# Performance work log

Measured on AMD Instinct MI355X. Metric: run time of the kernel, lower is better.

The kernel has to match this reference:

```python
import jax, jax.numpy as jnp
import numpy as np

HIDDEN = 1024
ATT_FEAT = 2048
EMBED = 512


def setup_inputs() -> dict:
    key = jax.random.key(0)
    k1, k2, k3, k4, k5, k6 = jax.random.split(key, 6)
    B, S, N = 16, 64, 196
    hidden = jax.random.normal(k1, (B, S, HIDDEN), dtype=jnp.float32)
    feats = jax.random.normal(k2, (B, N, ATT_FEAT), dtype=jnp.float32)
    att_mask = jax.random.randint(k3, (B, N), 0, 2, dtype=jnp.int32)
    # parameters (scaled like default torch Linear init)
    w_h = jax.random.normal(k4, (HIDDEN, EMBED), dtype=jnp.float32) / np.sqrt(HIDDEN)
    w_u = jax.random.normal(k5, (ATT_FEAT, EMBED), dtype=jnp.float32) / np.sqrt(ATT_FEAT)
    b = jnp.ones((EMBED,), dtype=jnp.float32)
    w = jax.random.normal(k6, (EMBED,), dtype=jnp.float32) / np.sqrt(EMBED)
    return {"hidden": hidden, "feats": feats, "att_mask": att_mask,
            "w_h": w_h, "w_u": w_u, "b": b, "w": w}


def reference(hidden, feats, att_mask, w_h, w_u, b, w):
    # hidden: [B,S,H], feats: [B,N,F], att_mask: [B,N]
    Wh = jnp.einsum('bsh,he->bse', hidden, w_h)          # [B,S,E]
    Uv = jnp.einsum('bnf,fe->bne', feats, w_u)           # [B,N,E] (feats repeat is redundant; same math)
    # additive attention energies: tanh(Wh + Uv + b) . w  -> [B,S,N]
    e = jnp.tanh(Wh[:, :, None, :] + Uv[:, None, :, :] + b)
    scores = jnp.einsum('bsne,e->bsn', e, w)             # [B,S,N]
    scores = jnp.where(att_mask[:, None, :] == 0, jnp.float32(-1e9), scores)
    weights = jax.nn.softmax(scores, axis=-1)            # [B,S,N]
    attn_feats = jnp.einsum('bsn,bnf->bsf', weights, feats)  # [B,S,F]
    return attn_feats, weights
```

## Files before the change

kernel.cpp:

```cpp
#include <hip/hip_runtime.h>
#include <math.h>

#define BATCH 16
#define SEQ 64
#define NKEY 196
#define NPAD 224
#define HIDDEN 1024
#define ATT_FEAT 2048
#define EMBED 512
#define MPAD 3200

using half8    = __attribute__((ext_vector_type(8))) _Float16;
using half4    = __attribute__((ext_vector_type(4))) _Float16;
using f32x4    = __attribute__((ext_vector_type(4))) float;
using f32x16   = __attribute__((ext_vector_type(16))) float;
using float4v  = __attribute__((ext_vector_type(4))) float;

#define KCONST (-2.8853900817779268f)
#define LOG2E  (1.4426950408889634f)

__device__ __forceinline__ void gl_lds16(const _Float16* g, _Float16* l) {
    __builtin_amdgcn_global_load_lds(
        (const __attribute__((address_space(1))) unsigned int*)g,
        (__attribute__((address_space(3))) unsigned int*)l, 16, 0, 0);
}

__device__ inline void prep_a128(
    const float* __restrict__ A, _Float16* __restrict__ T,
    int K, int Mreal, int tm, int tk, int t)
{
    const int r  = t >> 1;
    const int hf = t & 1;
    const int grow = tm * 128 + r;
    float f[32];
    if (grow < Mreal) {
        const float* src = A + (size_t)grow * K + tk * 64 + hf * 32;
        #pragma unroll
        for (int q = 0; q < 8; ++q) {
            float4v v = *(const float4v*)(src + q * 4);
            f[q*4+0] = v.x; f[q*4+1] = v.y; f[q*4+2] = v.z; f[q*4+3] = v.w;
        }
    } else {
        #pragma unroll
        for (int j = 0; j < 32; ++j) f[j] = 0.f;
    }
    const int tkk = tk * 2 + hf;
    const size_t base = ((size_t)tm * (K >> 5) + tkk) * 4096;
    #pragma unroll
    for (int s = 0; s < 2; ++s)
        #pragma unroll
        for (int kh = 0; kh < 2; ++kh) {
            half8 h;
            #pragma unroll
            for (int j = 0; j < 8; ++j)
                h[j] = (_Float16)f[s * 16 + kh * 8 + j];
            *(half8*)(T + base + (size_t)((s * 2 + kh) * 128 + r) * 8) = h;
        }
}

__device__ inline void prep_b128(
    const float* __restrict__ W, _Float16* __restrict__ T,
    int K, int N, int tn, int tk, int t, float (*tile)[129])
{
    {
        const int kr = t >> 2;
        const int nc = (t & 3) * 32;
        const float* src = W + (size_t)(tk * 64 + kr) * N + tn * 128 + nc;
        #pragma unroll
        for (int q = 0; q < 8; ++q) {
            float4v v = *(const float4v*)(src + q * 4);
            tile[kr][nc + q*4 + 0] = v.x; tile[kr][nc + q*4 + 1] = v.y;
            tile[kr][nc + q*4 + 2] = v.z; tile[kr][nc + q*4 + 3] = v.w;
        }
    }
    __syncthreads();
    {
        const int c  = t >> 1;
        const int hf = t & 1;
        const int tkk = tk * 2 + hf;
        const size_t base = ((size_t)tn * (K >> 5) + tkk) * 4096;
        #pragma unroll
        for (int s = 0; s < 2; ++s)
            #pragma unroll
            for (int kh = 0; kh < 2; ++kh) {
                half8 h;
                #pragma unroll
                for (int j = 0; j < 8; ++j)
                    h[j] = (_Float16)tile[hf * 32 + s * 16 + kh * 8 + j][c];
                *(half8*)(T + base + (size_t)((s * 2 + kh) * 128 + c) * 8) = h;
            }
    }
}

__device__ inline void prep_bT(
    const float* __restrict__ Wb, _Float16* __restrict__ T,
    int tn, int tk, int t, float (*tile)[129])
{
    {
        const int kr = t >> 2;
        const int nc = (t & 3) * 32;
        const int gn = tk * 64 + kr;
        #pragma unroll
        for (int q = 0; q < 8; ++q) {
            float4v v = {0.f, 0.f, 0.f, 0.f};
            if (gn < NKEY)
                v = *(const float4v*)(Wb + (size_t)gn * ATT_FEAT + tn * 128 + nc + q * 4);
            tile[kr][nc + q*4 + 0] = v.x; tile[kr][nc + q*4 + 1] = v.y;
            tile[kr][nc + q*4 + 2] = v.z; tile[kr][nc + q*4 + 3] = v.w;
        }
    }
    __syncthreads();
    {
        const int c  = t >> 1;
        const int hf = t & 1;
        const int tkk = tk * 2 + hf;
        if (tkk < 7) {
            const size_t base = ((size_t)tn * 7 + tkk) * 4096;
            #pragma unroll
            for (int s = 0; s < 2; ++s)
                #pragma unroll
                for (int kh = 0; kh < 2; ++kh) {
                    half8 h;
                    #pragma unroll
                    for (int j = 0; j < 8; ++j)
                        h[j] = (_Float16)tile[hf * 32 + s * 16 + kh * 8 + j][c];
                    *(half8*)(T + base + (size_t)((s * 2 + kh) * 128 + c) * 8) = h;
                }
        }
    }
}

__global__ __launch_bounds__(256) void uber_prep(
    const float* __restrict__ hidden, const float* __restrict__ feats,
    const float* __restrict__ w_h, const float* __restrict__ w_u,
    _Float16* HA, _Float16* FA, _Float16* HB, _Float16* UB)
{
    __shared__ float tile[64][129];
    const int id = blockIdx.x;
    const int t  = threadIdx.x;
    if (id < 128) {
        prep_a128(hidden, HA, HIDDEN, BATCH * SEQ, id >> 4, id & 15, t);
    } else if (id < 928) {
        const int j = id - 128;
        prep_a128(feats, FA, ATT_FEAT, BATCH * NKEY, j >> 5, j & 31, t);
    } else if (id < 992) {
        const int j = id - 928;
        prep_b128(w_h, HB, HIDDEN, EMBED, j >> 4, j & 15, t, tile);
    } else {
        const int j = id - 992;
        prep_b128(w_u, UB, ATT_FEAT, EMBED, j >> 5, j & 31, t, tile);
    }
}

__global__ __launch_bounds__(256) void uber_gemm(
    const _Float16* __restrict__ HA, const _Float16* __restrict__ HB,
    const _Float16* __restrict__ FA, const _Float16* __restrict__ UB,
    const float* __restrict__ bvec, _Float16* __restrict__ WhP,
    _Float16* __restrict__ UvP)
{
    __shared__ __align__(16) _Float16 L[2][3][4096];

    const int hh = blockIdx.x;
    const int t0 = (hh & 7) * 58 + (hh >> 3);

    const _Float16 *Aimg, *Bimg;
    const float* bias = nullptr;
    _Float16* C;
    int rt, ct, tk0, aK;
    if (t0 < 400) {
        const int ks = t0 / 100, rem = t0 % 100;
        rt = rem >> 2; ct = rem & 3;
        Aimg = FA; Bimg = UB;
        aK = ATT_FEAT >> 5; tk0 = ks * 16;
        C = UvP + (size_t)ks * MPAD * EMBED;
        if (ks == 0) bias = bvec;
    } else {
        const int v = t0 - 400;
        const int ks = v >> 5, rem = v & 31;
        rt = rem >> 2; ct = rem & 3;
        Aimg = HA; Bimg = HB;
        aK = HIDDEN >> 5; tk0 = ks * 16;
        C = WhP + (size_t)ks * (BATCH * SEQ) * EMBED;
    }

    const int tid = threadIdx.x, lane = tid & 63, w = tid >> 6;
    const int wr = w >> 1, wc = w & 1;
    const int l31 = lane & 31, kh = lane >> 5;

    const int isB = w >> 1;
    const int whf = w & 1;
    const _Float16* srcMat = isB ? Bimg : Aimg;
    const int majorTile = isB ? ct : rt;
    const _Float16* src0 =
        srcMat + ((size_t)majorTile * aK + tk0) * 4096 + whf * 2048 + lane * 8;

    f32x16 acc[2][2] = {};

    auto stage = [&](int buf, int t) {
        const _Float16* s = src0 + (size_t)t * 4096;
        _Float16* d = &L[isB][buf][0] + whf * 2048 + lane * 8;
        #pragma unroll
        for (int c = 0; c < 4; ++c)
            gl_lds16(s + c * 512, d + c * 512);
    };

    auto compute = [&](int buf) {
        #pragma unroll
        for (int s = 0; s < 2; ++s) {
            const int rb = (s * 2 + kh) * 128;
            half8 a[2], b[2];
            #pragma unroll
            for (int m = 0; m < 2; ++m)
                a[m] = *(const half8*)&L[0][buf][(rb + wr * 64 + m * 32 + l31) * 8];
            #pragma unroll
            for (int n = 0; n < 2; ++n)
                b[n] = *(const half8*)&L[1][buf][(rb + wc * 64 + n * 32 + l31) * 8];
            __builtin_amdgcn_s_setprio(1);
            #pragma unroll
            for (int m = 0; m < 2; ++m)
                #pragma unroll
                for (int n = 0; n < 2; ++n)
                    acc[m][n] = __builtin_amdgcn_mfma_f32_32x32x16_f16(a[m], b[n], acc[m][n], 0, 0, 0);
            __builtin_amdgcn_s_setprio(0);
        }
    };

    stage(0, 0); stage(1, 1);
    int cur = 0, nxt = 2;
    #pragma unroll 1
    for (int t = 0; t < 16; ++t) {
        if (t + 1 < 16) asm volatile("s_waitcnt vmcnt(4)" ::: "memory");
        else            asm volatile("s_waitcnt vmcnt(0)" ::: "memory");
        __builtin_amdgcn_s_barrier();
        if (t + 2 < 16) stage(nxt, t + 2);
        __builtin_amdgcn_sched_barrier(0);
        compute(cur);
        __builtin_amdgcn_sched_barrier(0);
        cur = (cur == 2) ? 0 : cur + 1;
        nxt = (nxt == 2) ? 0 : nxt + 1;
    }

    #pragma unroll
    for (int m = 0; m < 2; ++m) {
        const int row0 = rt * 128 + wr * 64 + m * 32;
        #pragma unroll
        for (int n = 0; n < 2; ++n) {
            const int colg = ct * 128 + wc * 64 + n * 32 + l31;
            const float bv = bias ? bias[colg] : 0.f;
            #pragma unroll
            for (int r = 0; r < 16; ++r) {
                const int row = (r & 3) + 8 * (r >> 2) + 4 * kh;
                C[(size_t)(row0 + row) * EMBED + colg] =
                    (_Float16)((acc[m][n][r] + bv) * KCONST);
            }
        }
    }
}

__global__ __launch_bounds__(256) void scores_ft(
    const _Float16* __restrict__ WhP, const _Float16* __restrict__ UvP,
    const float* __restrict__ wvec, const float* __restrict__ feats,
    float* __restrict__ scr4, _Float16* __restrict__ FT)
{
    __shared__ __align__(16) char smem[64 * 129 * 4];
    const int id = blockIdx.x;
    const int tid = threadIdx.x;

    if (id >= 832) {
        const int j = id - 832;
        const int b = j >> 6, rem = j & 63;
        prep_bT(feats + (size_t)b * NKEY * ATT_FEAT,
                FT + (size_t)b * 16 * 7 * 4096, rem >> 2, rem & 3, tid,
                (float(*)[129])smem);
        return;
    }

    const int n0 = (id % 13) * 16;
    const int eq = (id / 13) & 3;
    const int b  = id / 52;
    const int w    = tid >> 6;
    const int lane = tid & 63;

    float* whs = (float*)smem;
    float (*uvs)[64] = (float(*)[64])(smem + 16384);

    const size_t WHS = (size_t)(BATCH * SEQ) * EMBED;
    const size_t UVS = (size_t)MPAD * EMBED;

    float acc[4] = {};
    char* whsB = (char*)whs;

    for (int ch = 0; ch < 2; ++ch) {
        const int e0 = eq * 128 + ch * 64;
        {
            const int r = tid >> 2;
            const _Float16* Wr = WhP + (size_t)(b * SEQ + r) * EMBED + e0 + (tid & 3) * 16;
            half8 h0 = *(const half8*)(Wr);
            half8 h1 = *(const half8*)(Wr + 8);
            half8 g0 = *(const half8*)(Wr + WHS);
            half8 g1 = *(const half8*)(Wr + WHS + 8);
            float f[16];
            #pragma unroll
            for (int j = 0; j < 8; ++j) {
                f[j]     = (float)h0[j] + (float)g0[j];
                f[8 + j] = (float)h1[j] + (float)g1[j];
            }
            #pragma unroll
            for (int q = 0; q < 4; ++q) {
                const int cc = (tid & 3) * 16 + q * 4;
                float4v v = { f[q*4+0], f[q*4+1], f[q*4+2], f[q*4+3] };
                *(float4v*)(whsB + r * 256 + ((cc * 4) ^ ((r & 15) << 4))) = v;
            }
        }
        {
            const int nl = tid >> 4;
            const int c4 = tid & 15;
            const int nr = (n0 + nl < NKEY) ? (n0 + nl) : (NKEY - 1);
            const _Float16* Ur = UvP + (size_t)(b * NKEY + nr) * EMBED + e0 + c4 * 4;
            half4 u0 = *(const half4*)(Ur);
            half4 u1 = *(const half4*)(Ur + UVS);
            half4 u2 = *(const half4*)(Ur + 2 * UVS);
            half4 u3 = *(const half4*)(Ur + 3 * UVS);
            float4v u;
            u.x = ((float)u0[0] + (float)u1[0]) + ((float)u2[0] + (float)u3[0]);
            u.y = ((float)u0[1] + (float)u1[1]) + ((float)u2[1] + (float)u3[1]);
            u.z = ((float)u0[2] + (float)u1[2]) + ((float)u2[2] + (float)u3[2]);
            u.w = ((float)u0[3] + (float)u1[3]) + ((float)u2[3] + (float)u3[3]);
            *(float4v*)&uvs[nl][c4 * 4] = u;
        }
        __syncthreads();

        #pragma unroll
        for (int ec = 0; ec < 8; ++ec) {
            const int sb = lane * 256;
            float4v wh0 = *(const float4v*)(whsB + sb + ((ec * 32 +  0) ^ ((lane & 15) << 4)));
            float4v wh1 = *(const float4v*)(whsB + sb + ((ec * 32 + 16) ^ ((lane & 15) << 4)));
            float wf[8];
            #pragma unroll
            for (int i = 0; i < 8; ++i) wf[i] = wvec[e0 + ec * 8 + i];
            #pragma unroll
            for (int j = 0; j < 4; ++j) {
                const int nl = w * 4 + j;
                float4v u0 = *(const float4v*)&uvs[nl][ec * 8];
                float4v u1 = *(const float4v*)&uvs[nl][ec * 8 + 4];
                float t0 = __builtin_amdgcn_exp2f(wh0.x + u0.x);
                float t1 = __builtin_amdgcn_exp2f(wh0.y + u0.y);
                float t2 = __builtin_amdgcn_exp2f(wh0.z + u0.z);
                float t3 = __builtin_amdgcn_exp2f(wh0.w + u0.w);
                float t4 = __builtin_amdgcn_exp2f(wh1.x + u1.x);
                float t5 = __builtin_amdgcn_exp2f(wh1.y + u1.y);
                float t6 = __builtin_amdgcn_exp2f(wh1.z + u1.z);
                float t7 = __builtin_amdgcn_exp2f(wh1.w + u1.w);
                float a = acc[j];
                a = fmaf(wf[0], __builtin_amdgcn_rcpf(1.f + t0), a);
                a = fmaf(wf[1], __builtin_amdgcn_rcpf(1.f + t1), a);
                a = fmaf(wf[2], __builtin_amdgcn_rcpf(1.f + t2), a);
                a = fmaf(wf[3], __builtin_amdgcn_rcpf(1.f + t3), a);
                a = fmaf(wf[4], __builtin_amdgcn_rcpf(1.f + t4), a);
                a = fmaf(wf[5], __builtin_amdgcn_rcpf(1.f + t5), a);
                a = fmaf(wf[6], __builtin_amdgcn_rcpf(1.f + t6), a);
                a = fmaf(wf[7], __builtin_amdgcn_rcpf(1.f + t7), a);
                acc[j] = a;
            }
        }
        __syncthreads();
    }

    float* dst = scr4 + ((size_t)eq * (BATCH * SEQ) + b * SEQ + lane) * NKEY;
    #pragma unroll
    for (int j = 0; j < 4; ++j) {
        const int n = n0 + w * 4 + j;
        if (n < NKEY) dst[n] = 2.f * acc[j];
    }
}

__global__ __launch_bounds__(256) void attn_mfma(
    const float* __restrict__ scr4, const int* __restrict__ mask,
    const _Float16* __restrict__ FT,
    float* __restrict__ weights_out, float* __restrict__ out)
{
    const int fb = blockIdx.x;
    const int b  = blockIdx.y;
    const int t  = threadIdx.x;
    const int lane = t & 63, w = t >> 6;
    const int wr = w >> 1, wc = w & 1;
    const int l31 = lane & 31, khl = lane >> 5;

    __shared__ __align__(16) _Float16 wtL[7 * 4 * 64 * 8];
    __shared__ __align__(16) _Float16 Lb[3][4096];

    const _Float16* FTb = FT + (size_t)b * 16 * 7 * 4096 + (size_t)fb * 7 * 4096;

    auto stage = [&](int buf, int kt) {
        const _Float16* s = FTb + (size_t)kt * 4096 + w * 1024 + lane * 8;
        _Float16* d = &Lb[buf][0] + w * 1024 + lane * 8;
        gl_lds16(s, d);
        gl_lds16(s + 512, d + 512);
    };

    stage(0, 0); stage(1, 1);

    #pragma unroll
    for (int i = 0; i < 7; ++i)
        *(half8*)&wtL[(i * 256 + t) * 8] = (half8)(_Float16)0.f;

    asm volatile("s_waitcnt lgkmcnt(0)" ::: "memory");
    __builtin_amdgcn_s_barrier();

    {
        const int r  = t >> 2;
        const int ln = t & 3;
        const size_t SCRS = (size_t)(BATCH * SEQ) * NKEY;
        const float* p = scr4 + (size_t)(b * SEQ + r) * NKEY;
        const int* mrow = mask + b * NKEY;
        float v[49];
        float mx = -INFINITY;
        #pragma unroll
        for (int j = 0; j < 49; ++j) {
            const int n = ln + 4 * j;
            float s = (p[n] + p[SCRS + n]) + (p[2 * SCRS + n] + p[3 * SCRS + n]);
            if (mrow[n] == 0) s = -1e9f;
            v[j] = s;
            mx = fmaxf(mx, s);
        }
        mx = fmaxf(mx, __shfl_xor(mx, 1));
        mx = fmaxf(mx, __shfl_xor(mx, 2));
        float sum = 0.f;
        #pragma unroll
        for (int j = 0; j < 49; ++j) {
            v[j] = __builtin_amdgcn_exp2f((v[j] - mx) * LOG2E);
            sum += v[j];
        }
        sum += __shfl_xor(sum, 1);
        sum += __shfl_xor(sum, 2);
        const float inv = __builtin_amdgcn_rcpf(sum);
        float* wrow = weights_out + (size_t)(b * SEQ + r) * NKEY;
        #pragma unroll
        for (int j = 0; j < 49; ++j) {
            const int n = ln + 4 * j;
            const float wv = v[j] * inv;
            if (fb == 0) wrow[n] = wv;
            const int grp = ((n >> 4) & 1) * 2 + ((n >> 3) & 1);
            wtL[(((n >> 5) * 4 + grp) * 64 + r) * 8 + (n & 7)] = (_Float16)wv;
        }
    }
    asm volatile("s_waitcnt lgkmcnt(0)" ::: "memory");

    f32x16 acc[2] = {};
    #pragma unroll 1
    for (int kt = 0; kt < 7; ++kt) {
        if (kt < 6) asm volatile("s_waitcnt vmcnt(2)" ::: "memory");
        else        asm volatile("s_waitcnt vmcnt(0)" ::: "memory");
        __builtin_amdgcn_s_barrier();
        if (kt + 2 < 7) stage((kt + 2) % 3, kt + 2);
        __builtin_amdgcn_sched_barrier(0);
        const int buf = kt % 3;
        #pragma unroll
        for (int ks = 0; ks < 2; ++ks) {
            half8 a = *(const half8*)&wtL[(((kt * 4) + ks * 2 + khl) * 64 + wr * 32 + l31) * 8];
            half8 b0 = *(const half8*)&Lb[buf][((ks * 2 + khl) * 128 + wc * 64 + l31) * 8];
            half8 b1 = *(const half8*)&Lb[buf][((ks * 2 + khl) * 128 + wc * 64 + 32 + l31) * 8];
            acc[0] = __builtin_amdgcn_mfma_f32_32x32x16_f16(a, b0, acc[0], 0, 0, 0);
            acc[1] = __builtin_amdgcn_mfma_f32_32x32x16_f16(a, b1, acc[1], 0, 0, 0);
        }
        __builtin_amdgcn_sched_barrier(0);
    }

    #pragma unroll
    for (int nf = 0; nf < 2; ++nf) {
        const int f = fb * 128 + wc * 64 + nf * 32 + l31;
        #pragma unroll
        for (int r = 0; r < 16; ++r) {
            const int srow = wr * 32 + (r & 3) + 8 * (r >> 2) + 4 * khl;
            out[(size_t)(b * SEQ + srow) * ATT_FEAT + f] = acc[nf][r];
        }
    }
}

extern "C" void kernel_launch(void* const* d_in, const int* in_sizes, int n_in,
                              void* d_out, int out_size, void* d_ws, size_t ws_size,
                              hipStream_t stream)
{
    const float* hidden = (const float*)d_in[0];
    const float* feats  = (const float*)d_in[1];
    const int*   mask   = (const int*)  d_in[2];
    const float* w_h    = (const float*)d_in[3];
    const float* w_u    = (const float*)d_in[4];
    const float* bvec   = (const float*)d_in[5];
    const float* wvec   = (const float*)d_in[6];

    float* out         = (float*)d_out;
    float* attn_out    = out;
    float* weights_out = out + (size_t)BATCH * SEQ * ATT_FEAT;

    _Float16* WhP = (_Float16*)d_ws;
    _Float16* UvP = WhP + (size_t)2 * BATCH * SEQ * EMBED;
    float*    scr4 = (float*)(UvP + (size_t)4 * MPAD * EMBED);
    _Float16* FA = (_Float16*)(scr4 + (size_t)4 * BATCH * SEQ * NKEY);
    _Float16* HA = FA + (size_t)MPAD * ATT_FEAT;
    _Float16* UB = HA + (size_t)BATCH * SEQ * HIDDEN;
    _Float16* HB = UB + (size_t)EMBED * ATT_FEAT;
    _Float16* FT = HB + (size_t)EMBED * HIDDEN;

    uber_prep<<<dim3(1120), 256, 0, stream>>>(
        hidden, feats, w_h, w_u, HA, FA, HB, UB);

    uber_gemm<<<dim3(464), 256, 0, stream>>>(
        HA, HB, FA, UB, bvec, WhP, UvP);

    scores_ft<<<dim3(1856), 256, 0, stream>>>(
        WhP, UvP, wvec, feats, scr4, FT);

    attn_mfma<<<dim3(16, 16), 256, 0, stream>>>(
        scr4, mask, FT, weights_out, attn_out);
}
```

Measured before the change: 77.27 us.

## Fuse fp32-to-fp16 activation conversion into GEMM A-tile staging

Removes the separate prep pass that converted hidden and feats into packed fp16 tile images. The GEMM now loads fp32 A rows into registers, converts them and writes them to LDS itself, while B tiles still arrive through direct global-to-LDS loads. This saves a full write and reread of the fp16 activation copy. In exchange the pipeline drops from three LDS buffers to two, with register-staged prefetch and full __syncthreads barriers, and the A loads read twice as many bytes (fp32) inside the GEMM.

```diff
diff --git a/kernel.cpp b/kernel.cpp
--- a/kernel.cpp
+++ b/kernel.cpp
@@ -23,39 +23,6 @@
     __builtin_amdgcn_global_load_lds(
         (const __attribute__((address_space(1))) unsigned int*)g,
         (__attribute__((address_space(3))) unsigned int*)l, 16, 0, 0);
-}
-
-__device__ inline void prep_a128(
-    const float* __restrict__ A, _Float16* __restrict__ T,
-    int K, int Mreal, int tm, int tk, int t)
-{
-    const int r  = t >> 1;
-    const int hf = t & 1;
-    const int grow = tm * 128 + r;
-    float f[32];
-    if (grow < Mreal) {
-        const float* src = A + (size_t)grow * K + tk * 64 + hf * 32;
-        #pragma unroll
-        for (int q = 0; q < 8; ++q) {
-            float4v v = *(const float4v*)(src + q * 4);
-            f[q*4+0] = v.x; f[q*4+1] = v.y; f[q*4+2] = v.z; f[q*4+3] = v.w;
-        }
-    } else {
-        #pragma unroll
-        for (int j = 0; j < 32; ++j) f[j] = 0.f;
-    }
-    const int tkk = tk * 2 + hf;
-    const size_t base = ((size_t)tm * (K >> 5) + tkk) * 4096;
-    #pragma unroll
-    for (int s = 0; s < 2; ++s)
-        #pragma unroll
-        for (int kh = 0; kh < 2; ++kh) {
-            half8 h;
-            #pragma unroll
-            for (int j = 0; j < 8; ++j)
-                h[j] = (_Float16)f[s * 16 + kh * 8 + j];
-            *(half8*)(T + base + (size_t)((s * 2 + kh) * 128 + r) * 8) = h;
-        }
 }
 
 __device__ inline void prep_b128(
@@ -131,55 +98,52 @@
 }
 
 __global__ __launch_bounds__(256) void uber_prep(
-    const float* __restrict__ hidden, const float* __restrict__ feats,
     const float* __restrict__ w_h, const float* __restrict__ w_u,
-    _Float16* HA, _Float16* FA, _Float16* HB, _Float16* UB)
+    _Float16* HB, _Float16* UB)
 {
     __shared__ float tile[64][129];
     const int id = blockIdx.x;
     const int t  = threadIdx.x;
-    if (id < 128) {
-        prep_a128(hidden, HA, HIDDEN, BATCH * SEQ, id >> 4, id & 15, t);
-    } else if (id < 928) {
-        const int j = id - 128;
-        prep_a128(feats, FA, ATT_FEAT, BATCH * NKEY, j >> 5, j & 31, t);
-    } else if (id < 992) {
-        const int j = id - 928;
-        prep_b128(w_h, HB, HIDDEN, EMBED, j >> 4, j & 15, t, tile);
+    if (id < 64) {
+        prep_b128(w_h, HB, HIDDEN, EMBED, id >> 4, id & 15, t, tile);
     } else {
-        const int j = id - 992;
+        const int j = id - 64;
         prep_b128(w_u, UB, ATT_FEAT, EMBED, j >> 5, j & 31, t, tile);
     }
 }
 
 __global__ __launch_bounds__(256) void uber_gemm(
-    const _Float16* __restrict__ HA, const _Float16* __restrict__ HB,
-    const _Float16* __restrict__ FA, const _Float16* __restrict__ UB,
+    const float* __restrict__ hidden, const float* __restrict__ feats,
+    const _Float16* __restrict__ HB, const _Float16* __restrict__ UB,
     const float* __restrict__ bvec, _Float16* __restrict__ WhP,
     _Float16* __restrict__ UvP)
 {
-    __shared__ __align__(16) _Float16 L[2][3][4096];
+    __shared__ __align__(16) _Float16 LA[2][4096];
+    __shared__ __align__(16) _Float16 LB[2][4096];
 
     const int hh = blockIdx.x;
     const int t0 = (hh & 7) * 58 + (hh >> 3);
 
-    const _Float16 *Aimg, *Bimg;
+    const float* Asrc;
+    const _Float16* Bimg;
     const float* bias = nullptr;
     _Float16* C;
-    int rt, ct, tk0, aK;
+    int rt, ct, tk0, lda, Mreal, bkt;
     if (t0 < 400) {
         const int ks = t0 / 100, rem = t0 % 100;
         rt = rem >> 2; ct = rem & 3;
-        Aimg = FA; Bimg = UB;
-        aK = ATT_FEAT >> 5; tk0 = ks * 16;
+        Asrc = feats; lda = ATT_FEAT; Mreal = BATCH * NKEY;
+        Bimg = UB; bkt = ATT_FEAT >> 5;
+        tk0 = ks * 16;
         C = UvP + (size_t)ks * MPAD * EMBED;
         if (ks == 0) bias = bvec;
     } else {
         const int v = t0 - 400;
         const int ks = v >> 5, rem = v & 31;
         rt = rem >> 2; ct = rem & 3;
-        Aimg = HA; Bimg = HB;
-        aK = HIDDEN >> 5; tk0 = ks * 16;
+        Asrc = hidden; lda = HIDDEN; Mreal = BATCH * SEQ;
+        Bimg = HB; bkt = HIDDEN >> 5;
+        tk0 = ks * 16;
         C = WhP + (size_t)ks * (BATCH * SEQ) * EMBED;
     }
 
@@ -187,22 +151,48 @@
     const int wr = w >> 1, wc = w & 1;
     const int l31 = lane & 31, kh = lane >> 5;
 
-    const int isB = w >> 1;
-    const int whf = w & 1;
-    const _Float16* srcMat = isB ? Bimg : Aimg;
-    const int majorTile = isB ? ct : rt;
-    const _Float16* src0 =
-        srcMat + ((size_t)majorTile * aK + tk0) * 4096 + whf * 2048 + lane * 8;
+    const int ar  = tid >> 1;
+    const int ahf = tid & 1;
+    const int grow = rt * 128 + ar;
+    const bool avalid = grow < Mreal;
+    const float* Abase = Asrc + (size_t)grow * lda + tk0 * 32 + ahf * 16;
+
+    const _Float16* Bsrc0 =
+        Bimg + ((size_t)ct * bkt + tk0) * 4096 + w * 1024 + lane * 8;
+
+    float4v Ar[4];
+    auto loadA = [&](int t) {
+        if (avalid) {
+            const float* p = Abase + t * 32;
+            Ar[0] = *(const float4v*)(p);
+            Ar[1] = *(const float4v*)(p + 4);
+            Ar[2] = *(const float4v*)(p + 8);
+            Ar[3] = *(const float4v*)(p + 12);
+        } else {
+            float4v z = {0.f, 0.f, 0.f, 0.f};
+            Ar[0] = z; Ar[1] = z; Ar[2] = z; Ar[3] = z;
+        }
+    };
+    auto writeA = [&](int buf) {
+        half8 h0, h1;
+        #pragma unroll
+        for (int j = 0; j < 4; ++j) {
+            h0[j]     = (_Float16)Ar[0][j];
+            h0[4 + j] = (_Float16)Ar[1][j];
+            h1[j]     = (_Float16)Ar[2][j];
+            h1[4 + j] = (_Float16)Ar[3][j];
+        }
+        *(half8*)&LA[buf][(size_t)((ahf * 2 + 0) * 128 + ar) * 8] = h0;
+        *(half8*)&LA[buf][(size_t)((ahf * 2 + 1) * 128 + ar) * 8] = h1;
+    };
+    auto stageB = [&](int buf, int t) {
+        const _Float16* s = Bsrc0 + (size_t)t * 4096;
+        _Float16* d = &LB[buf][0] + w * 1024 + lane * 8;
+        gl_lds16(s, d);
+        gl_lds16(s + 512, d + 512);
+    };
 
     f32x16 acc[2][2] = {};
-
-    auto stage = [&](int buf, int t) {
-        const _Float16* s = src0 + (size_t)t * 4096;
-        _Float16* d = &L[isB][buf][0] + whf * 2048 + lane * 8;
-        #pragma unroll
-        for (int c = 0; c < 4; ++c)
-            gl_lds16(s + c * 512, d + c * 512);
-    };
 
     auto compute = [&](int buf) {
         #pragma unroll
@@ -211,10 +201,10 @@
             half8 a[2], b[2];
             #pragma unroll
             for (int m = 0; m < 2; ++m)
-                a[m] = *(const half8*)&L[0][buf][(rb + wr * 64 + m * 32 + l31) * 8];
+                a[m] = *(const half8*)&LA[buf][(size_t)(rb + wr * 64 + m * 32 + l31) * 8];
             #pragma unroll
             for (int n = 0; n < 2; ++n)
-                b[n] = *(const half8*)&L[1][buf][(rb + wc * 64 + n * 32 + l31) * 8];
+                b[n] = *(const half8*)&LB[buf][(size_t)(rb + wc * 64 + n * 32 + l31) * 8];
             __builtin_amdgcn_s_setprio(1);
             #pragma unroll
             for (int m = 0; m < 2; ++m)
@@ -225,19 +215,25 @@
         }
     };
 
-    stage(0, 0); stage(1, 1);
-    int cur = 0, nxt = 2;
+    loadA(0);
+    stageB(0, 0);
+    asm volatile("s_waitcnt vmcnt(2)" ::: "memory");
+    writeA(0);
+
+    int cur = 0;
     #pragma unroll 1
     for (int t = 0; t < 16; ++t) {
-        if (t + 1 < 16) asm volatile("s_waitcnt vmcnt(4)" ::: "memory");
-        else            asm volatile("s_waitcnt vmcnt(0)" ::: "memory");
-        __builtin_amdgcn_s_barrier();
-        if (t + 2 < 16) stage(nxt, t + 2);
-        __builtin_amdgcn_sched_barrier(0);
+        __syncthreads();
+        if (t + 1 < 16) {
+            loadA(t + 1);
+            stageB(cur ^ 1, t + 1);
+        }
         compute(cur);
-        __builtin_amdgcn_sched_barrier(0);
-        cur = (cur == 2) ? 0 : cur + 1;
-        nxt = (nxt == 2) ? 0 : nxt + 1;
+        if (t + 1 < 16) {
+            asm volatile("s_waitcnt vmcnt(2)" ::: "memory");
+            writeA(cur ^ 1);
+        }
+        cur ^= 1;
     }
 
     #pragma unroll
@@ -496,17 +492,14 @@
     _Float16* WhP = (_Float16*)d_ws;
     _Float16* UvP = WhP + (size_t)2 * BATCH * SEQ * EMBED;
     float*    scr4 = (float*)(UvP + (size_t)4 * MPAD * EMBED);
-    _Float16* FA = (_Float16*)(scr4 + (size_t)4 * BATCH * SEQ * NKEY);
-    _Float16* HA = FA + (size_t)MPAD * ATT_FEAT;
-    _Float16* UB = HA + (size_t)BATCH * SEQ * HIDDEN;
+    _Float16* UB = (_Float16*)(scr4 + (size_t)4 * BATCH * SEQ * NKEY);
     _Float16* HB = UB + (size_t)EMBED * ATT_FEAT;
     _Float16* FT = HB + (size_t)EMBED * HIDDEN;
 
-    uber_prep<<<dim3(1120), 256, 0, stream>>>(
-        hidden, feats, w_h, w_u, HA, FA, HB, UB);
+    uber_prep<<<dim3(192), 256, 0, stream>>>(w_h, w_u, HB, UB);
 
     uber_gemm<<<dim3(464), 256, 0, stream>>>(
-        HA, HB, FA, UB, bvec, WhP, UvP);
+        hidden, feats, HB, UB, bvec, WhP, UvP);
 
     scores_ft<<<dim3(1856), 256, 0, stream>>>(
         WhP, UvP, wvec, feats, scr4, FT);
```

New measurement: 78.51 us. About the same (+1.6%).

## Move feats transpose prep from scores kernel into GEMM launch

Applied to the files above, without the earlier changes.

Moves the feats-transpose (FT) preparation blocks out of the scores kernel and into the GEMM launch, as extra blocks that run after the GEMM tiles on each XCD. The memory-bound transpose can then overlap with the compute-bound GEMM tail, and the scores kernel becomes lighter. The GEMM's shared memory grows to hold the transpose staging buffer, which may lower GEMM occupancy.

```diff
diff --git a/kernel.cpp b/kernel.cpp
--- a/kernel.cpp
+++ b/kernel.cpp
@@ -4,7 +4,6 @@
 #define BATCH 16
 #define SEQ 64
 #define NKEY 196
-#define NPAD 224
 #define HIDDEN 1024
 #define ATT_FEAT 2048
 #define EMBED 512
@@ -155,13 +154,26 @@
 __global__ __launch_bounds__(256) void uber_gemm(
     const _Float16* __restrict__ HA, const _Float16* __restrict__ HB,
     const _Float16* __restrict__ FA, const _Float16* __restrict__ UB,
-    const float* __restrict__ bvec, _Float16* __restrict__ WhP,
-    _Float16* __restrict__ UvP)
-{
-    __shared__ __align__(16) _Float16 L[2][3][4096];
-
-    const int hh = blockIdx.x;
-    const int t0 = (hh & 7) * 58 + (hh >> 3);
+    const float* __restrict__ feats, const float* __restrict__ bvec,
+    _Float16* __restrict__ WhP, _Float16* __restrict__ UvP,
+    _Float16* __restrict__ FT)
+{
+    __shared__ __align__(16) char smem[49152];
+
+    const int tid = threadIdx.x;
+    const int hh  = blockIdx.x;
+    const int xcd = hh & 7, idx = hh >> 3;
+
+    if (idx >= 58) {
+        const int f = xcd * 128 + (idx - 58);
+        const int b = f >> 6, rem = f & 63;
+        prep_bT(feats + (size_t)b * NKEY * ATT_FEAT,
+                FT + (size_t)b * 16 * 7 * 4096, rem >> 2, rem & 3, tid,
+                (float(*)[129])smem);
+        return;
+    }
+
+    const int t0 = xcd * 58 + idx;
 
     const _Float16 *Aimg, *Bimg;
     const float* bias = nullptr;
@@ -183,7 +195,7 @@
         C = WhP + (size_t)ks * (BATCH * SEQ) * EMBED;
     }
 
-    const int tid = threadIdx.x, lane = tid & 63, w = tid >> 6;
+    const int lane = tid & 63, w = tid >> 6;
     const int wr = w >> 1, wc = w & 1;
     const int l31 = lane & 31, kh = lane >> 5;
 
@@ -194,27 +206,31 @@
     const _Float16* src0 =
         srcMat + ((size_t)majorTile * aK + tk0) * 4096 + whf * 2048 + lane * 8;
 
+    _Float16* Lp = (_Float16*)smem;
+
     f32x16 acc[2][2] = {};
 
     auto stage = [&](int buf, int t) {
         const _Float16* s = src0 + (size_t)t * 4096;
-        _Float16* d = &L[isB][buf][0] + whf * 2048 + lane * 8;
+        _Float16* d = Lp + (isB * 3 + buf) * 4096 + whf * 2048 + lane * 8;
         #pragma unroll
         for (int c = 0; c < 4; ++c)
             gl_lds16(s + c * 512, d + c * 512);
     };
 
     auto compute = [&](int buf) {
+        const _Float16* LAb = Lp + buf * 4096;
+        const _Float16* LBb = Lp + (3 + buf) * 4096;
         #pragma unroll
         for (int s = 0; s < 2; ++s) {
             const int rb = (s * 2 + kh) * 128;
             half8 a[2], b[2];
             #pragma unroll
             for (int m = 0; m < 2; ++m)
-                a[m] = *(const half8*)&L[0][buf][(rb + wr * 64 + m * 32 + l31) * 8];
+                a[m] = *(const half8*)(LAb + (size_t)(rb + wr * 64 + m * 32 + l31) * 8);
             #pragma unroll
             for (int n = 0; n < 2; ++n)
-                b[n] = *(const half8*)&L[1][buf][(rb + wc * 64 + n * 32 + l31) * 8];
+                b[n] = *(const half8*)(LBb + (size_t)(rb + wc * 64 + n * 32 + l31) * 8);
             __builtin_amdgcn_s_setprio(1);
             #pragma unroll
             for (int m = 0; m < 2; ++m)
@@ -257,32 +273,20 @@
     }
 }
 
-__global__ __launch_bounds__(256) void scores_ft(
+__global__ __launch_bounds__(256) void scores4_kernel(
     const _Float16* __restrict__ WhP, const _Float16* __restrict__ UvP,
-    const float* __restrict__ wvec, const float* __restrict__ feats,
-    float* __restrict__ scr4, _Float16* __restrict__ FT)
-{
-    __shared__ __align__(16) char smem[64 * 129 * 4];
+    const float* __restrict__ wvec, float* __restrict__ scr4)
+{
     const int id = blockIdx.x;
-    const int tid = threadIdx.x;
-
-    if (id >= 832) {
-        const int j = id - 832;
-        const int b = j >> 6, rem = j & 63;
-        prep_bT(feats + (size_t)b * NKEY * ATT_FEAT,
-                FT + (size_t)b * 16 * 7 * 4096, rem >> 2, rem & 3, tid,
-                (float(*)[129])smem);
-        return;
-    }
-
     const int n0 = (id % 13) * 16;
     const int eq = (id / 13) & 3;
     const int b  = id / 52;
+    const int tid = threadIdx.x;
     const int w    = tid >> 6;
     const int lane = tid & 63;
 
-    float* whs = (float*)smem;
-    float (*uvs)[64] = (float(*)[64])(smem + 16384);
+    __shared__ float whs[64 * 64];
+    __shared__ float uvs[16][64];
 
     const size_t WHS = (size_t)(BATCH * SEQ) * EMBED;
     const size_t UVS = (size_t)MPAD * EMBED;
@@ -505,11 +509,11 @@
     uber_prep<<<dim3(1120), 256, 0, stream>>>(
         hidden, feats, w_h, w_u, HA, FA, HB, UB);
 
-    uber_gemm<<<dim3(464), 256, 0, stream>>>(
-        HA, HB, FA, UB, bvec, WhP, UvP);
-
-    scores_ft<<<dim3(1856), 256, 0, stream>>>(
-        WhP, UvP, wvec, feats, scr4, FT);
+    uber_gemm<<<dim3(1488), 256, 0, stream>>>(
+        HA, HB, FA, UB, feats, bvec, WhP, UvP, FT);
+
+    scores4_kernel<<<dim3(832), 256, 0, stream>>>(
+        WhP, UvP, wvec, scr4);
 
     attn_mfma<<<dim3(16, 16), 256, 0, stream>>>(
         scr4, mask, FT, weights_out, attn_out);
```

Measured after the change: 80.26 us. 1.04x slower.
